# Performance work log

Measured on AMD Instinct MI355X. Metric: run time of the kernel, lower is better.

## Reference

```python
import jax, jax.numpy as jnp
import numpy as np

EMBED_DIM = 1024
NUM_HEADS = 16
HEAD_DIM = EMBED_DIM // NUM_HEADS


def setup_inputs() -> dict:
    key = jax.random.key(0)
    ks = jax.random.split(key, 7)
    B, N, C = 2, 2048, EMBED_DIM
    s = 1.0 / np.sqrt(C)
    return {
        "x": jax.random.normal(ks[0], (B, N, C), dtype=jnp.float32),
        "phase_signal": jax.random.uniform(ks[1], (B,), dtype=jnp.float32),
        "qkv_w": jax.random.normal(ks[2], (3 * C, C), dtype=jnp.float32) * s,
        "qkv_b": jnp.zeros((3 * C,), dtype=jnp.float32),
        "proj_w": jax.random.normal(ks[3], (C, C), dtype=jnp.float32) * s,
        "proj_b": jnp.zeros((C,), dtype=jnp.float32),
        "phase_weight": jnp.ones((NUM_HEADS,), dtype=jnp.float32),
    }


def reference(x, phase_signal, qkv_w, qkv_b, proj_w, proj_b, phase_weight):
    B, N, C = x.shape
    H, D = NUM_HEADS, HEAD_DIM
    # qkv projection: [B,N,3C] -> [3,B,H,N,D]
    qkv = (x @ qkv_w.T + qkv_b).reshape(B, N, 3, H, D)
    qkv = jnp.transpose(qkv, (2, 0, 3, 1, 4))
    q, k, v = qkv[0], qkv[1], qkv[2]
    attn = jnp.einsum("bhnd,bhmd->bhnm", q, k) * (D ** -0.5)
    # per-(batch, head) phase modulation applied before softmax
    phase_mod = phase_weight[None, :, None, None] * phase_signal[:, None, None, None]
    attn = attn * (1.0 + 0.2 * phase_mod)
    attn = jax.nn.softmax(attn, axis=-1)  # dropout is identity in eval mode
    out = jnp.einsum("bhnm,bhmd->bhnd", attn, v)
    out = jnp.transpose(out, (0, 2, 1, 3)).reshape(B, N, C)
    return out @ proj_w.T + proj_b
```

## Files before the change

kernel.cpp:

```cpp
#include <hip/hip_runtime.h>
#include <stdint.h>

#define NUM_H 16
#define HD    64
#define CDIM  1024
#define NSEQ  2048
#define NBATCH 2
#define LOG2E 1.4426950408889634f

typedef __attribute__((ext_vector_type(8))) short short8;
typedef __attribute__((ext_vector_type(4))) float f32x4;
typedef __attribute__((ext_vector_type(16))) float f32x16;
typedef __attribute__((ext_vector_type(4))) unsigned short ushort4v;
typedef __attribute__((ext_vector_type(4))) float float4v;
typedef __attribute__((ext_vector_type(2))) unsigned int u32x2;

__device__ __forceinline__ unsigned short f2bf(float f) {
    unsigned int u = __builtin_bit_cast(unsigned int, f);
    unsigned int r = u + 0x7fffu + ((u >> 16) & 1u);
    return (unsigned short)(r >> 16);
}

__device__ __forceinline__ unsigned int cvtpk(float a, float b) {
    unsigned int r;
    asm("v_cvt_pk_bf16_f32 %0, %1, %2" : "=v"(r) : "v"(a), "v"(b));
    return r;
}

__device__ __forceinline__ void plswap(unsigned int &a, unsigned int &b) {
    asm("v_permlane32_swap_b32 %0, %1" : "+v"(a), "+v"(b));
}

__device__ __forceinline__ void gload_lds16(const void* g, const void* l) {
    __builtin_amdgcn_global_load_lds(
        (const __attribute__((address_space(1))) unsigned int*)(unsigned long long)(uintptr_t)g,
        (__attribute__((address_space(3))) unsigned int*)(unsigned int)(uintptr_t)l,
        16, 0, 0);
}

__global__ void cvt_bf16_kernel(const float* __restrict__ in,
                                unsigned short* __restrict__ out, int n4) {
    int i = blockIdx.x * blockDim.x + threadIdx.x;
    if (i < n4) {
        float4v v = *(const float4v*)(in + (size_t)i * 4);
        ushort4v o;
        o[0] = f2bf(v[0]); o[1] = f2bf(v[1]); o[2] = f2bf(v[2]); o[3] = f2bf(v[3]);
        *(ushort4v*)(out + (size_t)i * 4) = o;
    }
}

__global__ __launch_bounds__(512, 2) void gemm_qkv(
    const unsigned short* __restrict__ A,
    const unsigned short* __restrict__ Bw,
    const float* __restrict__ bias,
    const float* __restrict__ ps,
    const float* __restrict__ pw,
    unsigned short* __restrict__ qb,
    unsigned short* __restrict__ kfrag,
    unsigned short* __restrict__ vfrag)
{
    __shared__ unsigned short lds[2][2][2][128][64];

    const int tid = threadIdx.x;
    const int wid = tid >> 6;
    const int lane = tid & 63;
    const int l15 = lane & 15, l4 = lane >> 4;
    const int wave_m = wid >> 2, wave_n = wid & 3;

    const int bm = blockIdx.x;
    const int bn = blockIdx.y;

    f32x4 acc[8][4];
    const f32x4 zero4 = {0.f, 0.f, 0.f, 0.f};
#pragma unroll
    for (int m = 0; m < 8; ++m)
#pragma unroll
        for (int n = 0; n < 4; ++n) acc[m][n] = zero4;

    const int jr = lane >> 3;
    const int jc = ((lane & 7) ^ jr) << 4;
    const char* aB = (const char*)A  + (size_t)(bm * 256) * 2048;
    const char* bB = (const char*)Bw + (size_t)(bn * 256) * 2048;

    auto stageH = [&](int t, int which) {
        const int buf = t & 1;
        const int op = which >> 1, hf = which & 1;
        const char* src = (op == 0) ? aB : bB;
        const int rowb = hf * 128 + wid * 16;
        const size_t k0b = (size_t)t * 128;
        char* dst = (char*)&lds[buf][op][hf][wid * 16][0];
#pragma unroll
        for (int i = 0; i < 2; ++i)
            gload_lds16(src + (size_t)(rowb + i * 8 + jr) * 2048 + k0b + jc,
                        dst + i * 1024);
    };

    const int swz = (l15 & 7) << 4;
    auto rdA = [&](int buf, int mq, int mp, int kk) -> short8 {
        return *(const short8*)((const char*)&lds[buf][0][wave_m][mq * 64 + mp * 16 + l15][0]
                                + ((kk * 64 + l4 * 16) ^ swz));
    };
    auto rdB = [&](int buf, int nq, int np, int kk) -> short8 {
        const int br = wave_n * 64 + nq * 32 + np * 16 + l15;
        return *(const short8*)((const char*)&lds[buf][1][br >> 7][br & 127][0]
                                + ((kk * 64 + l4 * 16) ^ swz));
    };

    stageH(0, 0); stageH(0, 1); stageH(0, 2); stageH(0, 3);
    stageH(1, 2); stageH(1, 3); stageH(1, 0); stageH(1, 1);
    asm volatile("s_waitcnt vmcnt(8)" ::: "memory");
    __builtin_amdgcn_s_barrier();

    for (int t = 0; t < 16; ++t) {
        const int buf = t & 1;
        short8 af[4][2], bf[2][2][2];

#pragma unroll
        for (int mp = 0; mp < 4; ++mp) {
            af[mp][0] = rdA(buf, 0, mp, 0); af[mp][1] = rdA(buf, 0, mp, 1);
        }
#pragma unroll
        for (int np = 0; np < 2; ++np) {
            bf[0][np][0] = rdB(buf, 0, np, 0); bf[0][np][1] = rdB(buf, 0, np, 1);
        }
        __builtin_amdgcn_s_barrier();
        __builtin_amdgcn_s_setprio(1);
#pragma unroll
        for (int mp = 0; mp < 4; ++mp)
#pragma unroll
            for (int np = 0; np < 2; ++np)
#pragma unroll
                for (int kk = 0; kk < 2; ++kk)
                    acc[mp][np] = __builtin_amdgcn_mfma_f32_16x16x32_bf16(
                        af[mp][kk], bf[0][np][kk], acc[mp][np], 0, 0, 0);
        __builtin_amdgcn_s_setprio(0);
        __builtin_amdgcn_s_barrier();

#pragma unroll
        for (int np = 0; np < 2; ++np) {
            bf[1][np][0] = rdB(buf, 1, np, 0); bf[1][np][1] = rdB(buf, 1, np, 1);
        }
        if (t < 14) stageH(t + 2, 2);
        __builtin_amdgcn_s_barrier();
        __builtin_amdgcn_s_setprio(1);
#pragma unroll
        for (int mp = 0; mp < 4; ++mp)
#pragma unroll
            for (int np = 0; np < 2; ++np)
#pragma unroll
                for (int kk = 0; kk < 2; ++kk)
                    acc[mp][2 + np] = __builtin_amdgcn_mfma_f32_16x16x32_bf16(
                        af[mp][kk], bf[1][np][kk], acc[mp][2 + np], 0, 0, 0);
        __builtin_amdgcn_s_setprio(0);
        __builtin_amdgcn_s_barrier();

#pragma unroll
        for (int mp = 0; mp < 4; ++mp) {
            af[mp][0] = rdA(buf, 1, mp, 0); af[mp][1] = rdA(buf, 1, mp, 1);
        }
        if (t < 14) stageH(t + 2, 3);
        __builtin_amdgcn_s_barrier();
        __builtin_amdgcn_s_setprio(1);
#pragma unroll
        for (int mp = 0; mp < 4; ++mp)
#pragma unroll
            for (int np = 0; np < 2; ++np)
#pragma unroll
                for (int kk = 0; kk < 2; ++kk)
                    acc[4 + mp][np] = __builtin_amdgcn_mfma_f32_16x16x32_bf16(
                        af[mp][kk], bf[0][np][kk], acc[4 + mp][np], 0, 0, 0);
        __builtin_amdgcn_s_setprio(0);
        __builtin_amdgcn_s_barrier();

        if (t < 14) { stageH(t + 2, 0); stageH(t + 2, 1); }
        __builtin_amdgcn_s_barrier();
        __builtin_amdgcn_s_setprio(1);
#pragma unroll
        for (int mp = 0; mp < 4; ++mp)
#pragma unroll
            for (int np = 0; np < 2; ++np)
#pragma unroll
                for (int kk = 0; kk < 2; ++kk)
                    acc[4 + mp][2 + np] = __builtin_amdgcn_mfma_f32_16x16x32_bf16(
                        af[mp][kk], bf[1][np][kk], acc[4 + mp][2 + np], 0, 0, 0);
        __builtin_amdgcn_s_setprio(0);
        if (t < 14)       { asm volatile("s_waitcnt vmcnt(8)" ::: "memory"); }
        else if (t == 14) { asm volatile("s_waitcnt vmcnt(0)" ::: "memory"); }
        __builtin_amdgcn_s_barrier();
    }

    const int col_base = bn * 256 + wave_n * 64;
    const int t3b = bn >> 2;
    const int bb = bm >> 3;
    const int nn0 = (bm & 7) * 256;
    char* tbc = (char*)&lds[0][0][0][0][0];

    __syncthreads();

    if (t3b == 0) {
#pragma unroll
        for (int n = 0; n < 4; ++n) {
            const int d = n * 16 + l15;
            const float bv = bias[col_base + n * 16 + l15];
#pragma unroll
            for (int m = 0; m < 8; ++m) {
#pragma unroll
                for (int r = 0; r < 4; ++r) {
                    const int tt = wave_m * 128 + m * 16 + l4 * 4 + r;
                    *(unsigned short*)(tbc + wave_n * 32768 + tt * 128 +
                                       ((d * 2) ^ ((tt & 7) << 4))) = f2bf(acc[m][n][r] + bv);
                }
            }
        }
        __syncthreads();
#pragma unroll
        for (int i = 0; i < 16; ++i) {
            const int hq = i >> 2, sub = i & 3;
            const int tt = sub * 64 + (tid >> 3);
            const int chunk = tid & 7;
            const short8 v = *(const short8*)(tbc + hq * 32768 + tt * 128 +
                                              ((chunk * 16) ^ ((tt & 7) << 4)));
            *(short8*)(qb + ((size_t)(bb * 16 + bn * 4 + hq) * 2048 + nn0 + tt) * 64 + chunk * 8) = v;
        }
    } else if (t3b == 1) {
        const float ps0 = ps[0], ps1 = ps[1];
        const int hh = (bn - 4) * 4 + wave_n;
        const float kf = 0.125f * LOG2E *
                         (1.f + 0.2f * pw[hh] * ((bb == 0) ? ps0 : ps1));
#pragma unroll
        for (int n = 0; n < 4; ++n) {
            const int hi_ = l15 >> 3, e = l15 & 7;
            const float bv = bias[col_base + n * 16 + l15];
#pragma unroll
            for (int m = 0; m < 8; ++m) {
#pragma unroll
                for (int r = 0; r < 4; ++r) {
                    const int tt = wave_m * 128 + m * 16 + l4 * 4 + r;
                    const int ti = tt >> 6, u = tt & 63;
                    const int s_ = u >> 5, l31_ = u & 31;
                    *(unsigned short*)(tbc + (((wave_n * 4 + ti) * 8 + s_ * 4 + n) << 10) +
                                       ((hi_ * 32 + l31_) << 4) + e * 2) =
                        f2bf((acc[m][n][r] + bv) * kf);
                }
            }
        }
        __syncthreads();
#pragma unroll
        for (int i = 0; i < 16; ++i) {
            const int hq = i >> 2, ti = i & 3;
            const short8 v = *(const short8*)(tbc + i * 8192 + tid * 16);
            *(short8*)(kfrag + ((size_t)(bb * 16 + (bn - 4) * 4 + hq) * 32 +
                                ((bm & 7) * 4 + ti)) * 4096 + tid * 8) = v;
        }
    } else {
#pragma unroll
        for (int n = 0; n < 4; ++n) {
            const int d = n * 16 + l15;
            const int dt_ = n >> 1, l31_ = d & 31;
            const float bv = bias[col_base + n * 16 + l15];
#pragma unroll
            for (int m = 0; m < 8; ++m) {
#pragma unroll
                for (int r = 0; r < 4; ++r) {
                    const int tt = wave_m * 128 + m * 16 + l4 * 4 + r;
                    const int ti = tt >> 6, u = tt & 63;
                    const int ks = u >> 4, hi_ = (u >> 3) & 1, e = u & 7;
                    *(unsigned short*)(tbc + (((wave_n * 4 + ti) * 8 + dt_ * 4 + ks) << 10) +
                                       ((hi_ * 32 + l31_) << 4) + e * 2) =
                        f2bf(acc[m][n][r] + bv);
                }
            }
        }
        __syncthreads();
#pragma unroll
        for (int i = 0; i < 16; ++i) {
            const int hq = i >> 2, ti = i & 3;
            const short8 v = *(const short8*)(tbc + i * 8192 + tid * 16);
            *(short8*)(vfrag + ((size_t)(bb * 16 + (bn - 8) * 4 + hq) * 32 +
                                ((bm & 7) * 4 + ti)) * 4096 + tid * 8) = v;
        }
    }
}

__global__ __launch_bounds__(256, 2) void gemm_proj(
    const unsigned short* __restrict__ A,
    const unsigned short* __restrict__ Bw,
    const float* __restrict__ bias,
    float* __restrict__ out)
{
    __shared__ unsigned short As[2][128 * 64];
    __shared__ unsigned short Bs[2][128 * 64];
    const int tid = threadIdx.x;
    const int wid = tid >> 6;
    const int lane = tid & 63;
    const int l15 = lane & 15, l4 = lane >> 4;
    const int bm = blockIdx.x, bn = blockIdx.y;
    const int wr = wid >> 1, wc = wid & 1;

    f32x4 acc[4][4];
    const f32x4 zero4 = {0.f, 0.f, 0.f, 0.f};
#pragma unroll
    for (int m = 0; m < 4; ++m)
#pragma unroll
        for (int n = 0; n < 4; ++n) acc[m][n] = zero4;

    const int jr = lane >> 3;
    const int jc = ((lane & 7) ^ jr) << 4;
    const char* aB = (const char*)A  + (size_t)(bm * 128) * 2048;
    const char* bB = (const char*)Bw + (size_t)(bn * 128) * 2048;

    auto stage = [&](int buf, int k0) {
#pragma unroll
        for (int i = 0; i < 4; ++i) {
            const int rowb = wid * 32 + i * 8;
            gload_lds16(aB + (size_t)(rowb + jr) * 2048 + k0 * 2 + jc,
                        (const char*)&As[buf][0] + rowb * 128);
            gload_lds16(bB + (size_t)(rowb + jr) * 2048 + k0 * 2 + jc,
                        (const char*)&Bs[buf][0] + rowb * 128);
        }
    };

    const int swz = (l15 & 7) << 4;

    stage(0, 0);
    for (int it = 0; it < 16; ++it) {
        const int buf = it & 1;
        __syncthreads();
        if (it < 15) stage(buf ^ 1, (it + 1) * 64);
#pragma unroll
        for (int kk = 0; kk < 2; ++kk) {
            short8 a[4], b[4];
#pragma unroll
            for (int m = 0; m < 4; ++m)
                a[m] = *(const short8*)((const char*)&As[buf][0] +
                        (wr * 64 + m * 16 + l15) * 128 + ((kk * 64 + l4 * 16) ^ swz));
#pragma unroll
            for (int n = 0; n < 4; ++n)
                b[n] = *(const short8*)((const char*)&Bs[buf][0] +
                        (wc * 64 + n * 16 + l15) * 128 + ((kk * 64 + l4 * 16) ^ swz));
            __builtin_amdgcn_s_setprio(1);
#pragma unroll
            for (int m = 0; m < 4; ++m)
#pragma unroll
                for (int n = 0; n < 4; ++n)
                    acc[m][n] = __builtin_amdgcn_mfma_f32_16x16x32_bf16(a[m], b[n], acc[m][n], 0, 0, 0);
            __builtin_amdgcn_s_setprio(0);
        }
    }

    const int row_base = bm * 128 + wr * 64;
    const int col_base = bn * 128 + wc * 64;
#pragma unroll
    for (int n = 0; n < 4; ++n) {
        const int col = col_base + n * 16 + l15;
        const float bv = bias[col];
#pragma unroll
        for (int m = 0; m < 4; ++m) {
#pragma unroll
            for (int r = 0; r < 4; ++r) {
                const int row = row_base + m * 16 + l4 * 4 + r;
                out[(size_t)row * 1024 + col] = acc[m][n][r] + bv;
            }
        }
    }
}

__global__ __launch_bounds__(256, 2) void attn_kernel(
    const unsigned short* __restrict__ qb,
    const unsigned short* __restrict__ kfrag,
    const unsigned short* __restrict__ vfrag,
    unsigned short* __restrict__ aout)
{
    __shared__ unsigned short KVs[2][2][4096];

    const int tid = threadIdx.x;
    const int w = tid >> 6;
    const int l = tid & 63;
    const int l31 = l & 31;
    const int hi = l >> 5;

    const int bid = blockIdx.y * 16 + blockIdx.x;
    const int wg = (bid & 7) * 64 + (bid >> 3);
    const int bh = wg >> 4;
    const int b = bh >> 4, h = bh & 15;
    const int q0 = (wg & 15) * 128 + w * 32;

    const char* qg = (const char*)(qb + (size_t)bh * 2048 * 64);
    const unsigned short* kg = kfrag + (size_t)bh * 32 * 4096;
    const unsigned short* vg = vfrag + (size_t)bh * 32 * 4096;

    short8 qf[4];
#pragma unroll
    for (int t = 0; t < 4; ++t)
        qf[t] = *(const short8*)(qg + (size_t)(q0 + l31) * 128 + t * 32 + hi * 16);

    f32x16 oacc[2];
#pragma unroll
    for (int dt = 0; dt < 2; ++dt)
#pragma unroll
        for (int r = 0; r < 16; ++r) oacc[dt][r] = 0.f;
    float lr = 0.f;

    auto stage = [&](int buf, int T) {
#pragma unroll
        for (int i = 0; i < 2; ++i) {
            const int c = w * 2 + i;
            gload_lds16(kg + (size_t)T * 4096 + c * 512 + l * 8, &KVs[buf][0][c * 512]);
            gload_lds16(vg + (size_t)T * 4096 + c * 512 + l * 8, &KVs[buf][1][c * 512]);
        }
    };

    stage(0, 0);
    __syncthreads();

    for (int it = 0; it < 32; ++it) {
        const int buf = it & 1;
        if (it < 31) stage(buf ^ 1, it + 1);

        const unsigned short* Kb = &KVs[buf][0][0];
        const unsigned short* Vb = &KVs[buf][1][0];

        f32x16 sa[2];
        __builtin_amdgcn_s_setprio(1);
#pragma unroll
        for (int s = 0; s < 2; ++s) {
#pragma unroll
            for (int r = 0; r < 16; ++r) sa[s][r] = 0.f;
#pragma unroll
            for (int t = 0; t < 4; ++t) {
                const short8 kf = *(const short8*)(Kb + (s * 4 + t) * 512 + l * 8);
                sa[s] = __builtin_amdgcn_mfma_f32_32x32x16_bf16(kf, qf[t], sa[s], 0, 0, 0);
            }
        }
        __builtin_amdgcn_s_setprio(0);

#pragma unroll
        for (int s = 0; s < 2; ++s)
#pragma unroll
            for (int r = 0; r < 16; ++r)
                sa[s][r] = __builtin_amdgcn_exp2f(sa[s][r] - 20.0f);

        float ts[16];
#pragma unroll
        for (int r = 0; r < 16; ++r) ts[r] = sa[0][r] + sa[1][r];
#pragma unroll
        for (int d = 8; d >= 1; d >>= 1)
#pragma unroll
            for (int r = 0; r < 8; ++r)
                if (r < d) ts[r] += ts[r + d];
        lr += ts[0] + __shfl_xor(ts[0], 32);

#pragma unroll
        for (int s = 0; s < 2; ++s) {
            unsigned int wv[8];
#pragma unroll
            for (int g = 0; g < 8; ++g)
                wv[g] = cvtpk(sa[s][g * 2], sa[s][g * 2 + 1]);
            plswap(wv[0], wv[2]); plswap(wv[1], wv[3]);
            plswap(wv[4], wv[6]); plswap(wv[5], wv[7]);
            union { unsigned int u[4]; short8 s8; } f0, f1;
            f0.u[0] = wv[0]; f0.u[1] = wv[1]; f0.u[2] = wv[2]; f0.u[3] = wv[3];
            f1.u[0] = wv[4]; f1.u[1] = wv[5]; f1.u[2] = wv[6]; f1.u[3] = wv[7];
            __builtin_amdgcn_s_setprio(1);
#pragma unroll
            for (int dt = 0; dt < 2; ++dt) {
                const short8 v0 = *(const short8*)(Vb + (dt * 4 + s * 2 + 0) * 512 + l * 8);
                oacc[dt] = __builtin_amdgcn_mfma_f32_32x32x16_bf16(v0, f0.s8, oacc[dt], 0, 0, 0);
                const short8 v1 = *(const short8*)(Vb + (dt * 4 + s * 2 + 1) * 512 + l * 8);
                oacc[dt] = __builtin_amdgcn_mfma_f32_32x32x16_bf16(v1, f1.s8, oacc[dt], 0, 0, 0);
            }
            __builtin_amdgcn_s_setprio(0);
        }
        __syncthreads();
    }

    const float inv = 1.0f / lr;
    char* outp = (char*)aout + ((size_t)(b * 2048 + q0 + l31) * 1024 + h * 64) * 2;
#pragma unroll
    for (int dt = 0; dt < 2; ++dt)
#pragma unroll
        for (int rg = 0; rg < 4; ++rg) {
            u32x2 pkd;
            pkd[0] = cvtpk(oacc[dt][rg * 4 + 0] * inv, oacc[dt][rg * 4 + 1] * inv);
            pkd[1] = cvtpk(oacc[dt][rg * 4 + 2] * inv, oacc[dt][rg * 4 + 3] * inv);
            *(u32x2*)(outp + (size_t)(dt * 32 + rg * 8 + hi * 4) * 2) = pkd;
        }
}

extern "C" void kernel_launch(void* const* d_in, const int* in_sizes, int n_in,
                              void* d_out, int out_size, void* d_ws, size_t ws_size,
                              hipStream_t stream) {
    const float* x      = (const float*)d_in[0];
    const float* ps     = (const float*)d_in[1];
    const float* qkv_w  = (const float*)d_in[2];
    const float* qkv_b  = (const float*)d_in[3];
    const float* proj_w = (const float*)d_in[4];
    const float* proj_b = (const float*)d_in[5];
    const float* pw     = (const float*)d_in[6];
    float* out = (float*)d_out;
    char* ws = (char*)d_ws;

    unsigned short* x_bf    = (unsigned short*)(ws);
    unsigned short* w1_bf   = (unsigned short*)(ws + (8u  << 20));
    unsigned short* wp_bf   = (unsigned short*)(ws + (14u << 20));
    unsigned short* qb      = (unsigned short*)(ws + (16u << 20));
    unsigned short* kfrag   = (unsigned short*)(ws + (24u << 20));
    unsigned short* vfrag   = (unsigned short*)(ws + (32u << 20));
    unsigned short* attn_bf = x_bf;

    cvt_bf16_kernel<<<4096, 256, 0, stream>>>(x,      x_bf,  1048576);
    cvt_bf16_kernel<<<3072, 256, 0, stream>>>(qkv_w,  w1_bf, 786432);
    cvt_bf16_kernel<<<1024, 256, 0, stream>>>(proj_w, wp_bf, 262144);

    gemm_qkv<<<dim3(16, 12), 512, 0, stream>>>(x_bf, w1_bf, qkv_b, ps, pw, qb, kfrag, vfrag);
    attn_kernel<<<dim3(16, 32), 256, 0, stream>>>(qb, kfrag, vfrag, attn_bf);
    gemm_proj<<<dim3(32, 8), 256, 0, stream>>>(attn_bf, wp_bf, proj_b, out);
}
```

Baseline: 110.1 us.

## Split attention over KV halves with combine pass, fuse conversion kernels

Attention work is split in two along the key/value sequence: each block handles 16 KV tiles instead of 32, which doubles the grid to 1024 blocks and raises the launch-bounds occupancy hint to 4 blocks per CU. Each half writes a normalised bf16 partial output plus its softmax denominator, and a new combine kernel merges the halves with weights l0/(l0+l1). The three fp32-to-bf16 conversion launches are merged into one. The split costs an extra kernel launch, extra global traffic for the partials, and an extra bf16 rounding step. The merge also appears to rely on the softmax having no running-max subtraction, since it combines the halves using only their denominators.

```diff
diff --git a/kernel.cpp b/kernel.cpp
--- a/kernel.cpp
+++ b/kernel.cpp
@@ -21,6 +21,10 @@
     return (unsigned short)(r >> 16);
 }
 
+__device__ __forceinline__ float bf2f(unsigned short u) {
+    return __builtin_bit_cast(float, (unsigned int)u << 16);
+}
+
 __device__ __forceinline__ unsigned int cvtpk(float a, float b) {
     unsigned int r;
     asm("v_cvt_pk_bf16_f32 %0, %1, %2" : "=v"(r) : "v"(a), "v"(b));
@@ -38,15 +42,21 @@
         16, 0, 0);
 }
 
-__global__ void cvt_bf16_kernel(const float* __restrict__ in,
-                                unsigned short* __restrict__ out, int n4) {
+__global__ void cvt_all_kernel(const float* __restrict__ x,
+                               const float* __restrict__ w1,
+                               const float* __restrict__ wp,
+                               unsigned short* __restrict__ xo,
+                               unsigned short* __restrict__ w1o,
+                               unsigned short* __restrict__ wpo) {
     int i = blockIdx.x * blockDim.x + threadIdx.x;
-    if (i < n4) {
-        float4v v = *(const float4v*)(in + (size_t)i * 4);
-        ushort4v o;
-        o[0] = f2bf(v[0]); o[1] = f2bf(v[1]); o[2] = f2bf(v[2]); o[3] = f2bf(v[3]);
-        *(ushort4v*)(out + (size_t)i * 4) = o;
-    }
+    const float* in; unsigned short* out;
+    if (i < 1048576)      { in = x;  out = xo; }
+    else if (i < 1835008) { in = w1; out = w1o; i -= 1048576; }
+    else                  { in = wp; out = wpo; i -= 1835008; }
+    float4v v = *(const float4v*)(in + (size_t)i * 4);
+    ushort4v o;
+    o[0] = f2bf(v[0]); o[1] = f2bf(v[1]); o[2] = f2bf(v[2]); o[3] = f2bf(v[3]);
+    *(ushort4v*)(out + (size_t)i * 4) = o;
 }
 
 __global__ __launch_bounds__(512, 2) void gemm_qkv(
@@ -365,11 +375,13 @@
     }
 }
 
-__global__ __launch_bounds__(256, 2) void attn_kernel(
+__global__ __launch_bounds__(256, 4) void attn_kernel(
     const unsigned short* __restrict__ qb,
     const unsigned short* __restrict__ kfrag,
     const unsigned short* __restrict__ vfrag,
-    unsigned short* __restrict__ aout)
+    unsigned short* __restrict__ o0,
+    unsigned short* __restrict__ o1,
+    float* __restrict__ lrb)
 {
     __shared__ unsigned short KVs[2][2][4096];
 
@@ -379,15 +391,17 @@
     const int l31 = l & 31;
     const int hi = l >> 5;
 
-    const int bid = blockIdx.y * 16 + blockIdx.x;
-    const int wg = (bid & 7) * 64 + (bid >> 3);
-    const int bh = wg >> 4;
+    const int bid = blockIdx.y * 32 + blockIdx.x;
+    const int wg = (bid & 7) * 128 + (bid >> 3);
+    const int bh = wg >> 5;
+    const int r5 = wg & 31;
+    const int qt = r5 >> 1, kvh = r5 & 1;
     const int b = bh >> 4, h = bh & 15;
-    const int q0 = (wg & 15) * 128 + w * 32;
+    const int q0 = qt * 128 + w * 32;
 
     const char* qg = (const char*)(qb + (size_t)bh * 2048 * 64);
-    const unsigned short* kg = kfrag + (size_t)bh * 32 * 4096;
-    const unsigned short* vg = vfrag + (size_t)bh * 32 * 4096;
+    const unsigned short* kg = kfrag + ((size_t)bh * 32 + kvh * 16) * 4096;
+    const unsigned short* vg = vfrag + ((size_t)bh * 32 + kvh * 16) * 4096;
 
     short8 qf[4];
 #pragma unroll
@@ -413,9 +427,9 @@
     stage(0, 0);
     __syncthreads();
 
-    for (int it = 0; it < 32; ++it) {
+    for (int it = 0; it < 16; ++it) {
         const int buf = it & 1;
-        if (it < 31) stage(buf ^ 1, it + 1);
+        if (it < 15) stage(buf ^ 1, it + 1);
 
         const unsigned short* Kb = &KVs[buf][0][0];
         const unsigned short* Vb = &KVs[buf][1][0];
@@ -475,7 +489,8 @@
     }
 
     const float inv = 1.0f / lr;
-    char* outp = (char*)aout + ((size_t)(b * 2048 + q0 + l31) * 1024 + h * 64) * 2;
+    unsigned short* ob = kvh ? o1 : o0;
+    char* outp = (char*)ob + ((size_t)(b * 2048 + q0 + l31) * 1024 + h * 64) * 2;
 #pragma unroll
     for (int dt = 0; dt < 2; ++dt)
 #pragma unroll
@@ -485,6 +500,30 @@
             pkd[1] = cvtpk(oacc[dt][rg * 4 + 2] * inv, oacc[dt][rg * 4 + 3] * inv);
             *(u32x2*)(outp + (size_t)(dt * 32 + rg * 8 + hi * 4) * 2) = pkd;
         }
+    if (hi == 0)
+        lrb[(kvh << 16) + (bh << 11) + q0 + l31] = lr;
+}
+
+__global__ void combine_kernel(unsigned short* __restrict__ o0,
+                               const unsigned short* __restrict__ o1,
+                               const float* __restrict__ lrb) {
+    const int idx = blockIdx.x * blockDim.x + threadIdx.x;
+    const size_t e0 = (size_t)idx * 8;
+    const int row = (int)(e0 >> 10);
+    const int col = (int)(e0 & 1023);
+    const int b = row >> 11, q = row & 2047, h = col >> 6;
+    const int bhq = ((b * 16 + h) << 11) + q;
+    const float l0 = lrb[bhq], l1 = lrb[65536 + bhq];
+    const float w0 = l0 / (l0 + l1);
+    const float w1 = 1.0f - w0;
+    short8 v0 = *(short8*)(o0 + e0);
+    const short8 v1 = *(const short8*)(o1 + e0);
+    short8 o;
+#pragma unroll
+    for (int j = 0; j < 8; ++j)
+        o[j] = (short)f2bf(bf2f((unsigned short)v0[j]) * w0 +
+                           bf2f((unsigned short)v1[j]) * w1);
+    *(short8*)(o0 + e0) = o;
 }
 
 extern "C" void kernel_launch(void* const* d_in, const int* in_sizes, int n_in,
@@ -506,13 +545,14 @@
     unsigned short* qb      = (unsigned short*)(ws + (16u << 20));
     unsigned short* kfrag   = (unsigned short*)(ws + (24u << 20));
     unsigned short* vfrag   = (unsigned short*)(ws + (32u << 20));
-    unsigned short* attn_bf = x_bf;
-
-    cvt_bf16_kernel<<<4096, 256, 0, stream>>>(x,      x_bf,  1048576);
-    cvt_bf16_kernel<<<3072, 256, 0, stream>>>(qkv_w,  w1_bf, 786432);
-    cvt_bf16_kernel<<<1024, 256, 0, stream>>>(proj_w, wp_bf, 262144);
-
+    unsigned short* o1      = (unsigned short*)(ws + (40u << 20));
+    unsigned short* o0      = x_bf;
+    float*          lrb     = (float*)w1_bf;
+    unsigned short* attn_bf = o0;
+
+    cvt_all_kernel<<<8192, 256, 0, stream>>>(x, qkv_w, proj_w, x_bf, w1_bf, wp_bf);
     gemm_qkv<<<dim3(16, 12), 512, 0, stream>>>(x_bf, w1_bf, qkv_b, ps, pw, qb, kfrag, vfrag);
-    attn_kernel<<<dim3(16, 32), 256, 0, stream>>>(qb, kfrag, vfrag, attn_bf);
+    attn_kernel<<<dim3(32, 32), 256, 0, stream>>>(qb, kfrag, vfrag, o0, o1, lrb);
+    combine_kernel<<<2048, 256, 0, stream>>>(o0, o1, lrb);
     gemm_proj<<<dim3(32, 8), 256, 0, stream>>>(attn_bf, wp_bf, proj_b, out);
 }
```

Measured after the change: 113.0 us. +2.6%, slower.
